# Kernel tuning notes

Measured on AMD Instinct MI355X. Metric: run time of the kernel, lower is better.

The kernel has to match this reference:

```python
import jax, jax.numpy as jnp
import numpy as np

EPS = 1e-3  # LayerNorm eps used in the torch module
S, R = 32, 32  # stoch_dim, stoch_rank


def ln(x, g, b):
    m = jnp.mean(x, -1, keepdims=True)
    v = jnp.var(x, -1, keepdims=True)
    return (x - m) / jnp.sqrt(v + EPS) * g + b


def setup_inputs() -> dict:
    key = jax.random.key(0)
    ks = jax.random.split(key, 16)
    T, B, E, A, D, H = 64, 64, 1024, 6, 2048, 1000
    def w(k, shape, s=0.02):
        return (jax.random.normal(k, shape) * s).astype(jnp.float32)
    return dict(
        embeds=jax.random.normal(ks[0], (T, B, E), jnp.float32),
        actions=jax.random.normal(ks[1], (T, B, A), jnp.float32),
        resets=jax.random.bernoulli(ks[2], 0.01, (T, B)),
        h0=jnp.zeros((B, D), jnp.float32),
        z0=jnp.zeros((B, S * R), jnp.float32),
        zw=w(ks[3], (S * R, H)), zb=jnp.zeros(H, jnp.float32),
        aw=w(ks[4], (A, H)),
        in_g=jnp.ones(H, jnp.float32), in_b=jnp.zeros(H, jnp.float32),
        gru_wi=w(ks[5], (H, 3 * D)), gru_wh=w(ks[6], (D, 3 * D)),
        gru_bi=jnp.zeros(3 * D, jnp.float32), gru_bh=jnp.zeros(3 * D, jnp.float32),
        ph_w=w(ks[7], (D, H)), ph_b=jnp.zeros(H, jnp.float32),
        pe_w=w(ks[8], (E, H)),
        po_g=jnp.ones(H, jnp.float32), po_b=jnp.zeros(H, jnp.float32),
        pp_w=w(ks[9], (H, S * R)), pp_b=jnp.zeros(S * R, jnp.float32),
        prh_w=w(ks[10], (D, H)), prh_b=jnp.zeros(H, jnp.float32),
        pr_g=jnp.ones(H, jnp.float32), pr_b=jnp.zeros(H, jnp.float32),
        prp_w=w(ks[11], (H, S * R)), prp_b=jnp.zeros(S * R, jnp.float32),
    )


def reference(embeds, actions, resets, h0, z0, zw, zb, aw, in_g, in_b,
              gru_wi, gru_wh, gru_bi, gru_bh, ph_w, ph_b, pe_w, po_g, po_b,
              pp_w, pp_b, prh_w, prh_b, pr_g, pr_b, prp_w, prp_b):
    T, B = embeds.shape[:2]
    base = jax.random.key(42)
    mask = (~resets)[..., None].astype(embeds.dtype)  # [T,B,1]

    def step(carry, xs):
        h, z = carry
        a, e, m, t = xs
        h = h * m
        z = z * m
        # input stage: z_mlp + a_mlp -> LN -> ELU
        x = jax.nn.elu(ln(z @ zw + zb + a @ aw, in_g, in_b))
        # single GRUCell (PyTorch gate order r, z, n)
        gi = x @ gru_wi + gru_bi
        gh = h @ gru_wh + gru_bh
        gir, giz, gin = jnp.split(gi, 3, -1)
        ghr, ghz, ghn = jnp.split(gh, 3, -1)
        r = jax.nn.sigmoid(gir + ghr)
        u = jax.nn.sigmoid(giz + ghz)
        n = jnp.tanh(gin + r * ghn)
        h = (1.0 - u) * n + u * h
        # posterior head (embed is provided every step)
        x = jax.nn.elu(ln(h @ ph_w + ph_b + e @ pe_w, po_g, po_b))
        pp = x @ pp_w + pp_b  # [B, S*R]
        logits = pp.reshape(B, S, R)
        probs = jax.nn.softmax(logits, -1)
        idx = jax.random.categorical(jax.random.fold_in(base, t), logits, axis=-1)
        oh = jax.nn.one_hot(idx, R, dtype=pp.dtype)
        # straight-through one-hot sample
        sample = (oh + probs - jax.lax.stop_gradient(probs)).reshape(B, S * R)
        return (h, sample), (pp, h, sample)

    (h_last, z_last), (posts, states_h, samples) = jax.lax.scan(
        step, (h0, z0), (actions, embeds, mask, jnp.arange(T)))
    # batch_prior over all timesteps at once
    priors = jax.nn.elu(ln(states_h @ prh_w + prh_b, pr_g, pr_b)) @ prp_w + prp_b
    features = jnp.concatenate([states_h, samples], -1)  # [T,B,3072]
    return priors, posts, samples, features, h_last, z_last
```

## Files before the change

### kernel.cpp

```cpp
#include <hip/hip_runtime.h>
#include <hip/hip_bf16.h>


#define BK 32
#define LDP 66
#define NBLK 512

enum { TR_NONE = 0, TR_SCALEROW = 1, TR_LNELU = 2 };

__device__ inline float cload(const float* p) {
  return __hip_atomic_load(p, __ATOMIC_RELAXED, __HIP_MEMORY_SCOPE_SYSTEM);
}
__device__ inline void cstore(float* p, float v) {
  __hip_atomic_store(p, v, __ATOMIC_RELAXED, __HIP_MEMORY_SCOPE_SYSTEM);
}
__device__ inline float2 cload2(const float* p) {
  unsigned long long u = __hip_atomic_load((const unsigned long long*)p,
                                           __ATOMIC_RELAXED, __HIP_MEMORY_SCOPE_SYSTEM);
  float2 r;
  r.x = __uint_as_float((unsigned)u);
  r.y = __uint_as_float((unsigned)(u >> 32));
  return r;
}
__device__ inline void cstore2(float* p, float x, float y) {
  unsigned long long u =
      ((unsigned long long)__float_as_uint(y) << 32) | (unsigned long long)__float_as_uint(x);
  __hip_atomic_store((unsigned long long*)p, u, __ATOMIC_RELAXED, __HIP_MEMORY_SCOPE_SYSTEM);
}
__device__ inline int cloadi(const int* p) {
  return __hip_atomic_load(p, __ATOMIC_RELAXED, __HIP_MEMORY_SCOPE_SYSTEM);
}
__device__ inline void cstorei(int* p, int v) {
  __hip_atomic_store(p, v, __ATOMIC_RELAXED, __HIP_MEMORY_SCOPE_SYSTEM);
}

__device__ inline float xla_tanh(float x) {
  float ax = fabsf(x);
  float xc = fminf(fmaxf(x, -7.90531110763549805f), 7.90531110763549805f);
  float x2 = __fmul_rn(xc, xc);
  float p = -2.76076847742355e-16f;
  p = __fadd_rn(__fmul_rn(p, x2), 2.00018790482477e-13f);
  p = __fadd_rn(__fmul_rn(p, x2), -8.60467152213735e-11f);
  p = __fadd_rn(__fmul_rn(p, x2), 5.12229709037114e-08f);
  p = __fadd_rn(__fmul_rn(p, x2), 1.48572235717979e-05f);
  p = __fadd_rn(__fmul_rn(p, x2), 6.37261928875436e-04f);
  p = __fadd_rn(__fmul_rn(p, x2), 4.89352455891786e-03f);
  float num = __fmul_rn(xc, p);
  float q = 1.19825839466702e-06f;
  q = __fadd_rn(__fmul_rn(q, x2), 1.18534705686654e-04f);
  q = __fadd_rn(__fmul_rn(q, x2), 2.26843463243900e-03f);
  q = __fadd_rn(__fmul_rn(q, x2), 4.89352518554385e-03f);
  float r = __fdiv_rn(num, q);
  return ax < 0.0004f ? x : r;
}

__device__ inline float sigm(float x) { return 1.0f / (1.0f + expf(-x)); }

__device__ inline void tfround(unsigned& x0, unsigned& x1, int r) {
  x0 += x1; x1 = (x1 << r) | (x1 >> (32 - r)); x1 ^= x0;
}
__device__ inline uint2 threefry(unsigned k0, unsigned k1, unsigned c0, unsigned c1) {
  unsigned ks2 = k0 ^ k1 ^ 0x1BD11BDAu;
  unsigned x0 = c0 + k0, x1 = c1 + k1;
  tfround(x0, x1, 13); tfround(x0, x1, 15); tfround(x0, x1, 26); tfround(x0, x1, 6);
  x0 += k1; x1 += ks2 + 1u;
  tfround(x0, x1, 17); tfround(x0, x1, 29); tfround(x0, x1, 16); tfround(x0, x1, 24);
  x0 += ks2; x1 += k0 + 2u;
  tfround(x0, x1, 13); tfround(x0, x1, 15); tfround(x0, x1, 26); tfround(x0, x1, 6);
  x0 += k0; x1 += k1 + 3u;
  tfround(x0, x1, 17); tfround(x0, x1, 29); tfround(x0, x1, 16); tfround(x0, x1, 24);
  x0 += k1; x1 += ks2 + 4u;
  tfround(x0, x1, 13); tfround(x0, x1, 15); tfround(x0, x1, 26); tfround(x0, x1, 6);
  x0 += ks2; x1 += k0 + 5u;
  return make_uint2(x0, x1);
}

struct GemmArgs {
  const float* A; int lda; const float* B; int ldb; int K; int ksplit;
  const float* A2; int lda2; const float* B2; int ldb2; int K2;
  int N; const float* bias;
  const float* t1s; const float* t1g; const float* t1b;
  float* C; int ldc; long partStride;
};

template <int TRA>
__device__ void gemm_tiles(float acc[4][4], float (*As)[LDP], float (*Bs)[LDP],
                           const float* A, int lda, const float* B, int ldb,
                           int kB, int kE, int mBase, int cBase, int N,
                           const float* s0, const float* g0, const float* b0) {
  const int tid = threadIdx.x;
  const int ar = tid >> 2;
  const int ak = (tid & 3) << 3;
  const int bk = tid >> 3;
  const int bc = (tid & 7) << 3;
  const int r0 = (tid >> 4) << 2;
  const int c0 = (tid & 15) << 2;

  float rowS = 1.f, rowM = 0.f, rowR = 1.f;
  if (TRA == TR_SCALEROW) rowS = s0[mBase + ar];
  else if (TRA == TR_LNELU) {
    rowM = s0[(mBase + ar) * 2];
    rowR = s0[(mBase + ar) * 2 + 1];
  }

  for (int kb = kB; kb < kE; kb += BK) {
    {
      const float* Ap = A + (long)(mBase + ar) * lda + kb + ak;
      float v[8];
      if (kb + ak + 7 < kE) {
        float4 u0 = *(const float4*)(Ap);
        float4 u1 = *(const float4*)(Ap + 4);
        v[0] = u0.x; v[1] = u0.y; v[2] = u0.z; v[3] = u0.w;
        v[4] = u1.x; v[5] = u1.y; v[6] = u1.z; v[7] = u1.w;
      } else {
#pragma unroll
        for (int i = 0; i < 8; i++) v[i] = (kb + ak + i < kE) ? Ap[i] : 0.f;
      }
#pragma unroll
      for (int i = 0; i < 8; i++) {
        int k = kb + ak + i;
        float x = 0.f;
        if (k < kE) {
          x = v[i];
          if (TRA == TR_SCALEROW) {
            x *= rowS;
          } else if (TRA == TR_LNELU) {
            x = (x - rowM) * rowR * g0[k] + b0[k];
            x = x > 0.f ? x : expm1f(x);
          }
        }
        As[ak + i][ar] = x;
      }
    }
    {
      int k = kb + bk;
      const float* Bp = B + (long)k * ldb + cBase + bc;
      if (k < kE && cBase + bc + 7 < N) {
        float4 u0 = *(const float4*)(Bp);
        float4 u1 = *(const float4*)(Bp + 4);
        Bs[bk][bc + 0] = u0.x; Bs[bk][bc + 1] = u0.y;
        Bs[bk][bc + 2] = u0.z; Bs[bk][bc + 3] = u0.w;
        Bs[bk][bc + 4] = u1.x; Bs[bk][bc + 5] = u1.y;
        Bs[bk][bc + 6] = u1.z; Bs[bk][bc + 7] = u1.w;
      } else {
#pragma unroll
        for (int i = 0; i < 8; i++)
          Bs[bk][bc + i] = (k < kE && cBase + bc + i < N) ? Bp[i] : 0.f;
      }
    }
    __syncthreads();
#pragma unroll
    for (int kk = 0; kk < BK; kk++) {
      float4 a4 = *(const float4*)&As[kk][r0];
      float4 b4 = *(const float4*)&Bs[kk][c0];
      float av[4] = {a4.x, a4.y, a4.z, a4.w};
      float bv[4] = {b4.x, b4.y, b4.z, b4.w};
#pragma unroll
      for (int i = 0; i < 4; i++)
#pragma unroll
        for (int j = 0; j < 4; j++) acc[i][j] += av[i] * bv[j];
    }
    __syncthreads();
  }
}

template <int TRA, int TRA2>
__global__ __launch_bounds__(256) void k_gemm(GemmArgs g) {
  __shared__ float As[BK][LDP];
  __shared__ float Bs[BK][LDP];
  const int nT = blockIdx.x, ks = blockIdx.y, mT = blockIdx.z;
  const int mBase = mT * 64, cBase = nT * 64;
  float acc[4][4] = {};
  int chunk = (((g.K + g.ksplit - 1) / g.ksplit) + 31) & ~31;
  int kB = ks * chunk, kE = min(g.K, kB + chunk);
  if (kB < kE)
    gemm_tiles<TRA>(acc, As, Bs, g.A, g.lda, g.B, g.ldb, kB, kE, mBase, cBase,
                    g.N, g.t1s, g.t1g, g.t1b);
  if (g.A2) {
    int chunk2 = (((g.K2 + g.ksplit - 1) / g.ksplit) + 31) & ~31;
    int kB2 = ks * chunk2, kE2 = min(g.K2, kB2 + chunk2);
    if (kB2 < kE2)
      gemm_tiles<TRA2>(acc, As, Bs, g.A2, g.lda2, g.B2, g.ldb2, kB2, kE2, mBase,
                       cBase, g.N, nullptr, nullptr, nullptr);
  }
  const int tid = threadIdx.x;
  const int r0 = (tid >> 4) << 2, c0 = (tid & 15) << 2;
  float* Cb = g.C + (long)ks * g.partStride;
#pragma unroll
  for (int i = 0; i < 4; i++) {
    float4 v = make_float4(acc[i][0], acc[i][1], acc[i][2], acc[i][3]);
    if (ks == 0 && g.bias) {
      int c = cBase + c0;
      v.x += (c + 0 < g.N) ? g.bias[c + 0] : 0.f;
      v.y += (c + 1 < g.N) ? g.bias[c + 1] : 0.f;
      v.z += (c + 2 < g.N) ? g.bias[c + 2] : 0.f;
      v.w += (c + 3 < g.N) ? g.bias[c + 3] : 0.f;
    }
    *(float4*)&Cb[(long)(mBase + r0 + i) * g.ldc + cBase + c0] = v;
  }
}

__global__ __launch_bounds__(256) void k_prstat(const float* xp, float* stats, int N) {
  int wave = threadIdx.x >> 6, lane = threadIdx.x & 63;
  int r = blockIdx.x * 4 + wave;
  float s = 0.f, sq = 0.f;
  for (int c = lane; c < N; c += 64) {
    float v = xp[(long)r * 1024 + c];
    s += v; sq += v * v;
  }
#pragma unroll
  for (int off = 32; off >= 1; off >>= 1) {
    s += __shfl_down(s, off);
    sq += __shfl_down(sq, off);
  }
  if (lane == 0) {
    float mean = s / N, var = sq / N - mean * mean;
    stats[r * 2] = mean;
    stats[r * 2 + 1] = 1.0f / sqrtf(var + 1e-3f);
  }
}

struct ScanArgs {
  const float* h0;
  const float* zw; const float* gwi; const float* gwh;
  const float* gbi; const float* gbh;
  const float* ph_w; const float* pp_w; const float* pp_b;
  const float* in_g; const float* in_b; const float* po_g; const float* po_b;
  const float* mask;
  const float* xa_base; const float* x2_base; const float* xa_t0;
  float* gi_parts; float* gh_parts; float* x2_parts; float* pp_parts;
  float* xe; float* x2e; int* idx;
  float* posts; float* samples; float* feats; float* hlast; float* zlast;
  unsigned* bar;
};

__device__ inline void gridbar(unsigned* bar, unsigned& lgen) {
  asm volatile("s_waitcnt vmcnt(0)" ::: "memory");
  __syncthreads();
  lgen++;
  if (threadIdx.x == 0) {
    int cell = (blockIdx.x & 7) * 32;
    unsigned prev = __hip_atomic_fetch_add(&bar[cell], 1u, __ATOMIC_RELAXED,
                                           __HIP_MEMORY_SCOPE_AGENT);
    if (prev == 64u * lgen - 1u) {
      unsigned p2 = __hip_atomic_fetch_add(&bar[256], 1u, __ATOMIC_RELAXED,
                                           __HIP_MEMORY_SCOPE_AGENT);
      if (p2 == 8u * lgen - 1u)
        __hip_atomic_store(&bar[288], lgen, __ATOMIC_RELAXED,
                           __HIP_MEMORY_SCOPE_AGENT);
    }
    while (__hip_atomic_load(&bar[288], __ATOMIC_RELAXED,
                             __HIP_MEMORY_SCOPE_AGENT) < lgen)
      __builtin_amdgcn_s_sleep(16);
  }
  __syncthreads();
}

template <int TRA>
__device__ void phase_gemm(float (*As)[LDP], float (*Bs)[LDP],
                           const float* A, int lda, const float* B, int ldb,
                           int kB, int kE, int cBase, int N,
                           const float* rowScale, float* C, int ldc,
                           const float* baseAdd, const float* colBias) {
  const int tid = threadIdx.x;
  const int ar = tid >> 2, ak = (tid & 3) << 3;
  const int bk = tid >> 3, bc = (tid & 7) << 3;
  const int r0 = (tid >> 4) << 2, c0 = (tid & 15) << 2;
  float acc[4][4] = {};
  float rowS = (TRA == TR_SCALEROW) ? rowScale[ar] : 1.f;

  for (int kb = kB; kb < kE; kb += BK) {
    float v[8];
    {
      const float* Ap = A + (long)ar * lda + kb + ak;
      if (kb + ak + 7 < kE) {
#pragma unroll
        for (int i = 0; i < 4; i++) {
          float2 u = cload2(Ap + 2 * i);
          v[2 * i] = u.x; v[2 * i + 1] = u.y;
        }
      } else {
#pragma unroll
        for (int i = 0; i < 8; i++) v[i] = (kb + ak + i < kE) ? cload(Ap + i) : 0.f;
      }
    }
    float w[8];
    {
      int k = kb + bk;
      const float* Bp = B + (long)k * ldb + cBase + bc;
      if (k < kE && cBase + bc + 7 < N) {
        float4 u0 = *(const float4*)(Bp);
        float4 u1 = *(const float4*)(Bp + 4);
        w[0] = u0.x; w[1] = u0.y; w[2] = u0.z; w[3] = u0.w;
        w[4] = u1.x; w[5] = u1.y; w[6] = u1.z; w[7] = u1.w;
      } else {
#pragma unroll
        for (int i = 0; i < 8; i++)
          w[i] = (k < kE && cBase + bc + i < N) ? Bp[i] : 0.f;
      }
    }
#pragma unroll
    for (int i = 0; i < 8; i++)
      As[ak + i][ar] = (TRA == TR_SCALEROW) ? v[i] * rowS : v[i];
#pragma unroll
    for (int i = 0; i < 8; i++) Bs[bk][bc + i] = w[i];
    __syncthreads();
#pragma unroll
    for (int kk = 0; kk < BK; kk++) {
      float4 a4 = *(const float4*)&As[kk][r0];
      float4 b4 = *(const float4*)&Bs[kk][c0];
      float av[4] = {a4.x, a4.y, a4.z, a4.w};
      float bv[4] = {b4.x, b4.y, b4.z, b4.w};
#pragma unroll
      for (int i = 0; i < 4; i++)
#pragma unroll
        for (int j = 0; j < 4; j++) acc[i][j] += av[i] * bv[j];
    }
    __syncthreads();
  }

#pragma unroll
  for (int i = 0; i < 4; i++) {
    float4 v4 = make_float4(acc[i][0], acc[i][1], acc[i][2], acc[i][3]);
    int c = cBase + c0;
    if (baseAdd) {
      const float* bp = baseAdd + (long)(r0 + i) * 1024 + c;
      v4.x += (c + 0 < N) ? bp[0] : 0.f;
      v4.y += (c + 1 < N) ? bp[1] : 0.f;
      v4.z += (c + 2 < N) ? bp[2] : 0.f;
      v4.w += (c + 3 < N) ? bp[3] : 0.f;
    }
    if (colBias) {
      v4.x += (c + 0 < N) ? colBias[c + 0] : 0.f;
      v4.y += (c + 1 < N) ? colBias[c + 1] : 0.f;
      v4.z += (c + 2 < N) ? colBias[c + 2] : 0.f;
      v4.w += (c + 3 < N) ? colBias[c + 3] : 0.f;
    }
    float* Cp = &C[(long)(r0 + i) * ldc + cBase + c0];
    cstore2(Cp, v4.x, v4.y);
    cstore2(Cp + 2, v4.z, v4.w);
  }
}

__device__ inline void ln_reduce(float s, float sq, float* red, float& mean,
                                 float& rstd) {
  const int tid = threadIdx.x;
#pragma unroll
  for (int off = 32; off >= 1; off >>= 1) {
    s += __shfl_down(s, off);
    sq += __shfl_down(sq, off);
  }
  if ((tid & 63) == 0) { red[tid >> 6] = s; red[4 + (tid >> 6)] = sq; }
  __syncthreads();
  if (tid == 0) {
    float S = red[0] + red[1] + red[2] + red[3];
    float Q = red[4] + red[5] + red[6] + red[7];
    float m = S / 1000.f;
    float var = Q / 1000.f - m * m;
    red[8] = m;
    red[9] = 1.f / sqrtf(var + 1e-3f);
  }
  __syncthreads();
  mean = red[8]; rstd = red[9];
}

__device__ void phase_p1(const ScanArgs& a, int t, float* red, int* gidx) {
  const int row = blockIdx.x, tid = threadIdx.x;
  if (t > 0 && tid < 32) gidx[tid] = cloadi(a.idx + row * 32 + tid);
  __syncthreads();
  float mk = a.mask[t * 64 + row];
  float v[4];
  float s = 0.f, sq = 0.f;
#pragma unroll
  for (int i = 0; i < 4; i++) {
    int c = tid + (i << 8);
    float x = 0.f;
    if (c < 1000) {
      if (t == 0) {
        x = a.xa_t0[row * 1024 + c];
      } else {
        float g = 0.f;
#pragma unroll
        for (int s2 = 0; s2 < 32; s2++)
          g += a.zw[(s2 * 32 + gidx[s2]) * 1000 + c];
        x = g * mk + a.xa_base[(long)t * 65536 + row * 1024 + c];
      }
      s += x; sq += x * x;
    }
    v[i] = x;
  }
  float mean, rstd;
  ln_reduce(s, sq, red, mean, rstd);
#pragma unroll
  for (int i = 0; i < 4; i++) {
    int c = tid + (i << 8);
    float y = 0.f;
    if (c < 1000) {
      y = (v[i] - mean) * rstd * a.in_g[c] + a.in_b[c];
      y = y > 0.f ? y : expm1f(y);
    }
    cstore(a.xe + row * 1024 + c, y);
  }
  __syncthreads();
}

__device__ void phase_p5(const ScanArgs& a, float* red) {
  const int row = blockIdx.x, tid = threadIdx.x;
  float v[4];
  float s = 0.f, sq = 0.f;
#pragma unroll
  for (int i = 0; i < 4; i++) {
    int c = tid + (i << 8);
    float x = 0.f;
    if (c < 1000) {
#pragma unroll
      for (int q = 0; q < 8; q++)
        x += cload(a.x2_parts + (long)q * 65536 + row * 1024 + c);
      s += x; sq += x * x;
    }
    v[i] = x;
  }
  float mean, rstd;
  ln_reduce(s, sq, red, mean, rstd);
#pragma unroll
  for (int i = 0; i < 4; i++) {
    int c = tid + (i << 8);
    float y = 0.f;
    if (c < 1000) {
      y = (v[i] - mean) * rstd * a.po_g[c] + a.po_b[c];
      y = y > 0.f ? y : expm1f(y);
    }
    cstore(a.x2e + row * 1024 + c, y);
  }
  __syncthreads();
}

__device__ void phase_gates(const ScanArgs& a, const float* hprev, int ldh,
                            const float* mk, float* feat_t, int t) {
  int p = blockIdx.x * 256 + threadIdx.x;
  int b = p >> 10, d = (p & 1023) << 1;
  long gio = (long)b * 6144 + d;
  float r0, r1, z0, z1, n0, n1;
  {
    float2 t0 = cload2(a.gi_parts + gio);
    float2 t1 = cload2(a.gi_parts + gio + 2048);
    float2 t2 = cload2(a.gi_parts + gio + 4096);
    r0 = t0.x; r1 = t0.y; z0 = t1.x; z1 = t1.y; n0 = t2.x; n1 = t2.y;
  }
#pragma unroll
  for (int q = 1; q < 5; q++) {
    long o = (long)q * 393216 + gio;
    float2 t0 = cload2(a.gi_parts + o);
    float2 t1 = cload2(a.gi_parts + o + 2048);
    float2 t2 = cload2(a.gi_parts + o + 4096);
    r0 += t0.x; r1 += t0.y; z0 += t1.x; z1 += t1.y; n0 += t2.x; n1 += t2.y;
  }
  r0 += a.gbi[d]; r1 += a.gbi[d + 1];
  z0 += a.gbi[d + 2048]; z1 += a.gbi[d + 2049];
  n0 += a.gbi[d + 4096]; n1 += a.gbi[d + 4097];
  float hr0 = a.gbh[d], hr1 = a.gbh[d + 1];
  float hz0 = a.gbh[d + 2048], hz1 = a.gbh[d + 2049];
  float hn0 = a.gbh[d + 4096], hn1 = a.gbh[d + 4097];
#pragma unroll
  for (int q = 0; q < 8; q++) {
    long o = (long)q * 393216 + gio;
    float2 t0 = cload2(a.gh_parts + o);
    float2 t1 = cload2(a.gh_parts + o + 2048);
    float2 t2 = cload2(a.gh_parts + o + 4096);
    hr0 += t0.x; hr1 += t0.y; hz0 += t1.x; hz1 += t1.y; hn0 += t2.x; hn1 += t2.y;
  }
  float2 hp = cload2(hprev + (long)b * ldh + d);
  float m = mk[b];
  float rr0 = sigm(r0 + hr0), rr1 = sigm(r1 + hr1);
  float uu0 = sigm(z0 + hz0), uu1 = sigm(z1 + hz1);
  float nn0 = xla_tanh(n0 + rr0 * hn0), nn1 = xla_tanh(n1 + rr1 * hn1);
  float h0v = (1.f - uu0) * nn0 + uu0 * (hp.x * m);
  float h1v = (1.f - uu1) * nn1 + uu1 * (hp.y * m);
  cstore2(feat_t + (long)b * 3072 + d, h0v, h1v);
  if (t == 63) {
    a.hlast[(long)b * 2048 + d] = h0v;
    a.hlast[(long)b * 2048 + d + 1] = h1v;
  }
}

__device__ void phase_sample(const ScanArgs& a, int t, float* feat_t) {
  int gid = blockIdx.x * 256 + threadIdx.x;
  int b = gid >> 10, sj = gid & 1023, j = sj & 31, sg = sj >> 5;
  float v = 0.f;
#pragma unroll
  for (int q = 0; q < 8; q++)
    v += cload(a.pp_parts + (long)q * 65536 + (long)b * 1024 + sj);
  a.posts[(long)t * 65536 + (long)b * 1024 + sj] = v;
  uint2 kt = threefry(0u, 42u, 0u, (unsigned)t);
  unsigned idx = (unsigned)(b * 1024 + sj);
  uint2 o = threefry(kt.x, kt.y, 0u, idx);
  unsigned bits = o.x ^ o.y;
  const float TINY = 1.175494350822287508e-38f;
  float u = __uint_as_float((bits >> 9) | 0x3f800000u) - 1.0f;
  u = fmaxf(TINY, u + TINY);
  float sc = v + -logf(-logf(u));
  float bs = sc;
  int bj = j;
#pragma unroll
  for (int off = 16; off >= 1; off >>= 1) {
    float os = __shfl_xor(bs, off, 32);
    int oj = __shfl_xor(bj, off, 32);
    if (os > bs || (os == bs && oj < bj)) { bs = os; bj = oj; }
  }
  float oh = (j == bj) ? 1.f : 0.f;
  a.samples[(long)t * 65536 + (long)b * 1024 + sj] = oh;
  feat_t[(long)b * 3072 + 2048 + sj] = oh;
  if (j == 0) cstorei(a.idx + b * 32 + sg, bj);
  if (t == 63) a.zlast[b * 1024 + sj] = oh;
}

__global__ __launch_bounds__(256, 2) void k_scan(ScanArgs a) {
  __shared__ float As[BK][LDP];
  __shared__ float Bs[BK][LDP];
  __shared__ float red[16];
  __shared__ int gidx[32];
  unsigned lgen = 0;
  const int bid = blockIdx.x;

  for (int half = 0; half < 2; half++) {
    if (bid >= 128) {
      int i2 = bid - 128;
      int tile = i2 % 96, ks = half * 4 + i2 / 96;
      phase_gemm<TR_SCALEROW>(As, Bs, a.h0, 2048, a.gwh, 6144, ks * 256,
                              ks * 256 + 256, tile * 64, 6144, a.mask,
                              a.gh_parts + (long)ks * 393216, 6144, nullptr,
                              nullptr);
    }
    gridbar(a.bar, lgen);
  }

  for (int t = 0; t < 64; t++) {
    const float* mk = a.mask + t * 64;
    float* feat_t = a.feats + (long)t * 196608;
    const float* hprev = t ? a.feats + (long)(t - 1) * 196608 : a.h0;
    int ldh = t ? 3072 : 2048;

    if (bid < 64) phase_p1(a, t, red, gidx);
    gridbar(a.bar, lgen);

    if (bid < 480) {
      int tile = bid % 96, ks = bid / 96;
      phase_gemm<TR_NONE>(As, Bs, a.xe, 1024, a.gwi, 6144, ks * 200,
                          ks * 200 + 200, tile * 64, 6144, nullptr,
                          a.gi_parts + (long)ks * 393216, 6144, nullptr, nullptr);
    }
    gridbar(a.bar, lgen);

    if (bid < 256) phase_gates(a, hprev, ldh, mk, feat_t, t);
    gridbar(a.bar, lgen);

    if (bid < 128) {
      int ct = bid & 15, ks = bid >> 4;
      phase_gemm<TR_NONE>(As, Bs, feat_t, 3072, a.ph_w, 1000, ks * 256,
                          ks * 256 + 256, ct * 64, 1000, nullptr,
                          a.x2_parts + (long)ks * 65536, 1024,
                          (ks == 0) ? a.x2_base + (long)t * 65536 : nullptr,
                          nullptr);
    } else if (t < 63) {
      int i2 = bid - 128;
      int tile = i2 % 96, ks = i2 / 96;
      phase_gemm<TR_SCALEROW>(As, Bs, feat_t, 3072, a.gwh, 6144, ks * 256,
                              ks * 256 + 256, tile * 64, 6144,
                              a.mask + (t + 1) * 64,
                              a.gh_parts + (long)ks * 393216, 6144, nullptr,
                              nullptr);
    }
    gridbar(a.bar, lgen);

    if (bid < 64) phase_p5(a, red);
    gridbar(a.bar, lgen);

    if (bid < 128) {
      int ct = bid & 15, ks = bid >> 4;
      int kB = ks * 128, kE = min(1000, kB + 128);
      phase_gemm<TR_NONE>(As, Bs, a.x2e, 1024, a.pp_w, 1024, kB, kE, ct * 64,
                          1024, nullptr, a.pp_parts + (long)ks * 65536, 1024,
                          nullptr, (ks == 0) ? a.pp_b : nullptr);
    } else if (t < 63) {
      int i2 = bid - 128;
      int tile = i2 % 96, ks = 4 + i2 / 96;
      phase_gemm<TR_SCALEROW>(As, Bs, feat_t, 3072, a.gwh, 6144, ks * 256,
                              ks * 256 + 256, tile * 64, 6144,
                              a.mask + (t + 1) * 64,
                              a.gh_parts + (long)ks * 393216, 6144, nullptr,
                              nullptr);
    }
    gridbar(a.bar, lgen);

    if (bid < 256) phase_sample(a, t, feat_t);
    gridbar(a.bar, lgen);
  }
}

__global__ void k_init(unsigned* bar) {
  int i = threadIdx.x;
  if (i < 512) bar[i] = 0u;
}

__global__ void k_detect(const unsigned* rr, int nDwordsSafe, int* fmt) {
  __shared__ int flags;
  if (threadIdx.x == 0) flags = 0;
  __syncthreads();
  int local = 0;
  for (int i = threadIdx.x; i < nDwordsSafe; i += 256) {
    unsigned dw = rr[i];
    if (dw == 0x3f800000u) local |= 4;
    else if (dw & 0xFFFFFF00u) local |= 1;
    else if (dw == 1u) local |= 2;
  }
  atomicOr(&flags, local);
  __syncthreads();
  if (threadIdx.x == 0) {
    int f = flags;
    *fmt = ((f & 4) == 0 && (f & 1)) ? 1 : 0;
  }
}

__global__ void k_prep(const void* rr, const int* fmt, float* mask, int n) {
  int i = blockIdx.x * 256 + threadIdx.x;
  if (i < n) {
    bool reset;
    if (*fmt == 1) reset = ((const unsigned char*)rr)[i] != 0;
    else reset = ((const int*)rr)[i] != 0;
    mask[i] = reset ? 0.0f : 1.0f;
  }
}

__global__ __launch_bounds__(256) void k_abase(const float* act, const float* aw,
                                               const float* zb, float* out) {
  for (long i = blockIdx.x * 256L + threadIdx.x; i < 4096L * 1024;
       i += (long)gridDim.x * 256) {
    int row = (int)(i >> 10), c = (int)(i & 1023);
    float v = 0.f;
    if (c < 1000) {
      v = zb[c];
#pragma unroll
      for (int k = 0; k < 6; k++) v += act[row * 6 + k] * aw[k * 1000 + c];
    }
    out[i] = v;
  }
}

extern "C" void kernel_launch(void* const* d_in, const int* in_sizes, int n_in,
                              void* d_out, int out_size, void* d_ws, size_t ws_size,
                              hipStream_t stream) {
  const float* embeds = (const float*)d_in[0];
  const float* actions = (const float*)d_in[1];
  const void* resets = d_in[2];
  const float* h0 = (const float*)d_in[3];
  const float* z0 = (const float*)d_in[4];
  const float* zw = (const float*)d_in[5];
  const float* zb = (const float*)d_in[6];
  const float* aw = (const float*)d_in[7];
  const float* in_g = (const float*)d_in[8];
  const float* in_b = (const float*)d_in[9];
  const float* gwi = (const float*)d_in[10];
  const float* gwh = (const float*)d_in[11];
  const float* gbi = (const float*)d_in[12];
  const float* gbh = (const float*)d_in[13];
  const float* ph_w = (const float*)d_in[14];
  const float* ph_b = (const float*)d_in[15];
  const float* pe_w = (const float*)d_in[16];
  const float* po_g = (const float*)d_in[17];
  const float* po_b = (const float*)d_in[18];
  const float* pp_w = (const float*)d_in[19];
  const float* pp_b = (const float*)d_in[20];
  const float* prh_w = (const float*)d_in[21];
  const float* prh_b = (const float*)d_in[22];
  const float* pr_g = (const float*)d_in[23];
  const float* pr_b = (const float*)d_in[24];
  const float* prp_w = (const float*)d_in[25];
  const float* prp_b = (const float*)d_in[26];

  float* out = (float*)d_out;
  float* priors  = out;
  float* posts   = out + 4194304;
  float* samples = out + 8388608;
  float* feats   = out + 12582912;
  float* hlast   = out + 25165824;
  float* zlast   = out + 25296896;

  float* ws = (float*)d_ws;
  unsigned* bar   = (unsigned*)ws;
  int*   fmt      = (int*)(ws + 512);
  float* mask     = ws + 576;
  float* stats_p  = ws + 4672;
  float* xe       = ws + 12864;
  float* x2e      = ws + 78400;
  int*   idxb     = (int*)(ws + 143936);
  float* xa_t0    = ws + 146048;
  float* gi_parts = ws + 211584;
  float* gh_parts = ws + 2177664;
  float* x2_parts = ws + 5323392;
  float* pp_parts = ws + 5847680;
  float* xa_base  = ws + 6371968;
  float* x2_base  = ws + 10566272;
  float* xp       = ws + 14760576;

  k_init<<<1, 512, 0, stream>>>(bar);
  k_detect<<<1, 256, 0, stream>>>((const unsigned*)resets, 1024, fmt);
  k_prep<<<16, 256, 0, stream>>>(resets, fmt, mask, 4096);
  k_abase<<<2048, 256, 0, stream>>>(actions, aw, zb, xa_base);

  GemmArgs g0{};
  g0.A = z0; g0.lda = 1024; g0.B = zw; g0.ldb = 1000; g0.K = 1024; g0.ksplit = 1;
  g0.A2 = actions; g0.lda2 = 6; g0.B2 = aw; g0.ldb2 = 1000; g0.K2 = 6;
  g0.N = 1000; g0.bias = zb; g0.t1s = mask;
  g0.C = xa_t0; g0.ldc = 1024; g0.partStride = 0;
  k_gemm<TR_SCALEROW, TR_NONE><<<dim3(16, 1, 1), 256, 0, stream>>>(g0);

  GemmArgs ge{};
  ge.A = embeds; ge.lda = 1024; ge.B = pe_w; ge.ldb = 1000; ge.K = 1024; ge.ksplit = 1;
  ge.N = 1000; ge.bias = ph_b; ge.C = x2_base; ge.ldc = 1024; ge.partStride = 0;
  k_gemm<TR_NONE, TR_NONE><<<dim3(16, 1, 64), 256, 0, stream>>>(ge);

  ScanArgs sa{};
  sa.h0 = h0; sa.zw = zw; sa.gwi = gwi; sa.gwh = gwh;
  sa.gbi = gbi; sa.gbh = gbh; sa.ph_w = ph_w; sa.pp_w = pp_w; sa.pp_b = pp_b;
  sa.in_g = in_g; sa.in_b = in_b; sa.po_g = po_g; sa.po_b = po_b;
  sa.mask = mask; sa.xa_base = xa_base; sa.x2_base = x2_base; sa.xa_t0 = xa_t0;
  sa.gi_parts = gi_parts; sa.gh_parts = gh_parts;
  sa.x2_parts = x2_parts; sa.pp_parts = pp_parts;
  sa.xe = xe; sa.x2e = x2e; sa.idx = idxb;
  sa.posts = posts; sa.samples = samples; sa.feats = feats;
  sa.hlast = hlast; sa.zlast = zlast; sa.bar = bar;
  k_scan<<<NBLK, 256, 0, stream>>>(sa);

  GemmArgs gp1{};
  gp1.A = feats; gp1.lda = 3072; gp1.B = prh_w; gp1.ldb = 1000; gp1.K = 2048; gp1.ksplit = 1;
  gp1.N = 1000; gp1.bias = prh_b; gp1.C = xp; gp1.ldc = 1024; gp1.partStride = 0;
  k_gemm<TR_NONE, TR_NONE><<<dim3(16, 1, 64), 256, 0, stream>>>(gp1);
  k_prstat<<<1024, 256, 0, stream>>>(xp, stats_p, 1000);
  GemmArgs gp2{};
  gp2.A = xp; gp2.lda = 1024; gp2.B = prp_w; gp2.ldb = 1024; gp2.K = 1000; gp2.ksplit = 1;
  gp2.N = 1024; gp2.bias = prp_b; gp2.t1s = stats_p; gp2.t1g = pr_g; gp2.t1b = pr_b;
  gp2.C = priors; gp2.ldc = 1024; gp2.partStride = 0;
  k_gemm<TR_LNELU, TR_NONE><<<dim3(16, 1, 64), 256, 0, stream>>>(gp2);
}
```

Before: 19.42 ms.

## Rebalance persistent scan phases with fewer split-K parts and fused posterior sampling

Restructures the per-timestep schedule of the persistent scan kernel. Split-K partition counts for the input-gate, hidden-gate and posterior-head GEMMs drop (5→2, 8→4, 8→4), so the gate and LayerNorm phases reduce fewer partial buffers. The next step's hidden-gate GEMM is spread across four phases, including the input-gate phase. The posterior logits GEMM is fused with Gumbel-max sampling in one tiled phase, which removes the pp_parts buffer and a grid barrier per step. It also adds register prefetch (software pipelining) to the shared GEMM loop and shortens the barrier spin sleep. In exchange, each active block does more serial K work and fewer blocks are busy in some phases.

```diff
diff --git a/kernel.cpp b/kernel.cpp
--- a/kernel.cpp
+++ b/kernel.cpp
@@ -228,7 +228,9 @@
   const float* in_g; const float* in_b; const float* po_g; const float* po_b;
   const float* mask;
   const float* xa_base; const float* x2_base; const float* xa_t0;
-  float* gi_parts; float* gh_parts; float* x2_parts; float* pp_parts;
+  float* gi_p;
+  float* gh_p;
+  float* x2_p;
   float* xe; float* x2e; int* idx;
   float* posts; float* samples; float* feats; float* hlast; float* zlast;
   unsigned* bar;
@@ -242,7 +244,7 @@
     int cell = (blockIdx.x & 7) * 32;
     unsigned prev = __hip_atomic_fetch_add(&bar[cell], 1u, __ATOMIC_RELAXED,
                                            __HIP_MEMORY_SCOPE_AGENT);
-    if (prev == 64u * lgen - 1u) {
+    if (prev == (unsigned)(NBLK / 8) * lgen - 1u) {
       unsigned p2 = __hip_atomic_fetch_add(&bar[256], 1u, __ATOMIC_RELAXED,
                                            __HIP_MEMORY_SCOPE_AGENT);
       if (p2 == 8u * lgen - 1u)
@@ -251,7 +253,7 @@
     }
     while (__hip_atomic_load(&bar[288], __ATOMIC_RELAXED,
                              __HIP_MEMORY_SCOPE_AGENT) < lgen)
-      __builtin_amdgcn_s_sleep(16);
+      __builtin_amdgcn_s_sleep(8);
   }
   __syncthreads();
 }
@@ -268,43 +270,45 @@
   const int r0 = (tid >> 4) << 2, c0 = (tid & 15) << 2;
   float acc[4][4] = {};
   float rowS = (TRA == TR_SCALEROW) ? rowScale[ar] : 1.f;
-
+  float v[8], w[8];
+
+  auto ldA = [&](int kb) {
+    const float* Ap = A + (long)ar * lda + kb + ak;
+    if (kb + ak + 7 < kE) {
+#pragma unroll
+      for (int i = 0; i < 4; i++) {
+        float2 u = cload2(Ap + 2 * i);
+        v[2 * i] = u.x; v[2 * i + 1] = u.y;
+      }
+    } else {
+#pragma unroll
+      for (int i = 0; i < 8; i++) v[i] = (kb + ak + i < kE) ? cload(Ap + i) : 0.f;
+    }
+  };
+  auto ldB = [&](int kb) {
+    int k = kb + bk;
+    const float* Bp = B + (long)k * ldb + cBase + bc;
+    if (k < kE && cBase + bc + 7 < N) {
+      float4 u0 = *(const float4*)(Bp);
+      float4 u1 = *(const float4*)(Bp + 4);
+      w[0] = u0.x; w[1] = u0.y; w[2] = u0.z; w[3] = u0.w;
+      w[4] = u1.x; w[5] = u1.y; w[6] = u1.z; w[7] = u1.w;
+    } else {
+#pragma unroll
+      for (int i = 0; i < 8; i++)
+        w[i] = (k < kE && cBase + bc + i < N) ? Bp[i] : 0.f;
+    }
+  };
+
+  ldA(kB); ldB(kB);
   for (int kb = kB; kb < kE; kb += BK) {
-    float v[8];
-    {
-      const float* Ap = A + (long)ar * lda + kb + ak;
-      if (kb + ak + 7 < kE) {
-#pragma unroll
-        for (int i = 0; i < 4; i++) {
-          float2 u = cload2(Ap + 2 * i);
-          v[2 * i] = u.x; v[2 * i + 1] = u.y;
-        }
-      } else {
-#pragma unroll
-        for (int i = 0; i < 8; i++) v[i] = (kb + ak + i < kE) ? cload(Ap + i) : 0.f;
-      }
-    }
-    float w[8];
-    {
-      int k = kb + bk;
-      const float* Bp = B + (long)k * ldb + cBase + bc;
-      if (k < kE && cBase + bc + 7 < N) {
-        float4 u0 = *(const float4*)(Bp);
-        float4 u1 = *(const float4*)(Bp + 4);
-        w[0] = u0.x; w[1] = u0.y; w[2] = u0.z; w[3] = u0.w;
-        w[4] = u1.x; w[5] = u1.y; w[6] = u1.z; w[7] = u1.w;
-      } else {
-#pragma unroll
-        for (int i = 0; i < 8; i++)
-          w[i] = (k < kE && cBase + bc + i < N) ? Bp[i] : 0.f;
-      }
-    }
 #pragma unroll
     for (int i = 0; i < 8; i++)
       As[ak + i][ar] = (TRA == TR_SCALEROW) ? v[i] * rowS : v[i];
 #pragma unroll
     for (int i = 0; i < 8; i++) Bs[bk][bc + i] = w[i];
     __syncthreads();
+    if (kb + BK < kE) { ldA(kb + BK); ldB(kb + BK); }
 #pragma unroll
     for (int kk = 0; kk < BK; kk++) {
       float4 a4 = *(const float4*)&As[kk][r0];
@@ -404,7 +408,7 @@
   __syncthreads();
 }
 
-__device__ void phase_p5(const ScanArgs& a, float* red) {
+__device__ void phase_x2e(const ScanArgs& a, float* red) {
   const int row = blockIdx.x, tid = threadIdx.x;
   float v[4];
   float s = 0.f, sq = 0.f;
@@ -414,8 +418,8 @@
     float x = 0.f;
     if (c < 1000) {
 #pragma unroll
-      for (int q = 0; q < 8; q++)
-        x += cload(a.x2_parts + (long)q * 65536 + row * 1024 + c);
+      for (int q = 0; q < 4; q++)
+        x += cload(a.x2_p + (long)q * 65536 + row * 1024 + c);
       s += x; sq += x * x;
     }
     v[i] = x;
@@ -440,19 +444,13 @@
   int p = blockIdx.x * 256 + threadIdx.x;
   int b = p >> 10, d = (p & 1023) << 1;
   long gio = (long)b * 6144 + d;
-  float r0, r1, z0, z1, n0, n1;
-  {
-    float2 t0 = cload2(a.gi_parts + gio);
-    float2 t1 = cload2(a.gi_parts + gio + 2048);
-    float2 t2 = cload2(a.gi_parts + gio + 4096);
-    r0 = t0.x; r1 = t0.y; z0 = t1.x; z1 = t1.y; n0 = t2.x; n1 = t2.y;
-  }
-#pragma unroll
-  for (int q = 1; q < 5; q++) {
+  float r0 = 0.f, r1 = 0.f, z0 = 0.f, z1 = 0.f, n0 = 0.f, n1 = 0.f;
+#pragma unroll
+  for (int q = 0; q < 2; q++) {
     long o = (long)q * 393216 + gio;
-    float2 t0 = cload2(a.gi_parts + o);
-    float2 t1 = cload2(a.gi_parts + o + 2048);
-    float2 t2 = cload2(a.gi_parts + o + 4096);
+    float2 t0 = cload2(a.gi_p + o);
+    float2 t1 = cload2(a.gi_p + o + 2048);
+    float2 t2 = cload2(a.gi_p + o + 4096);
     r0 += t0.x; r1 += t0.y; z0 += t1.x; z1 += t1.y; n0 += t2.x; n1 += t2.y;
   }
   r0 += a.gbi[d]; r1 += a.gbi[d + 1];
@@ -462,11 +460,11 @@
   float hz0 = a.gbh[d + 2048], hz1 = a.gbh[d + 2049];
   float hn0 = a.gbh[d + 4096], hn1 = a.gbh[d + 4097];
 #pragma unroll
-  for (int q = 0; q < 8; q++) {
+  for (int q = 0; q < 4; q++) {
     long o = (long)q * 393216 + gio;
-    float2 t0 = cload2(a.gh_parts + o);
-    float2 t1 = cload2(a.gh_parts + o + 2048);
-    float2 t2 = cload2(a.gh_parts + o + 4096);
+    float2 t0 = cload2(a.gh_p + o);
+    float2 t1 = cload2(a.gh_p + o + 2048);
+    float2 t2 = cload2(a.gh_p + o + 4096);
     hr0 += t0.x; hr1 += t0.y; hz0 += t1.x; hz1 += t1.y; hn0 += t2.x; hn1 += t2.y;
   }
   float2 hp = cload2(hprev + (long)b * ldh + d);
@@ -483,35 +481,93 @@
   }
 }
 
-__device__ void phase_sample(const ScanArgs& a, int t, float* feat_t) {
-  int gid = blockIdx.x * 256 + threadIdx.x;
-  int b = gid >> 10, sj = gid & 1023, j = sj & 31, sg = sj >> 5;
-  float v = 0.f;
-#pragma unroll
-  for (int q = 0; q < 8; q++)
-    v += cload(a.pp_parts + (long)q * 65536 + (long)b * 1024 + sj);
-  a.posts[(long)t * 65536 + (long)b * 1024 + sj] = v;
+__device__ void phase_pp(const ScanArgs& a, int t, int rg, int sg,
+                         float* As2, float* Bs2) {
+  const int tid = threadIdx.x;
+  const int ar = tid >> 3;
+  const int ak = (tid & 7) << 2;
+  const int bk = tid >> 3;
+  const int bc = (tid & 7) << 2;
+  const int rowBase = rg * 32, colBase = sg * 32;
+  float acc[4] = {0.f, 0.f, 0.f, 0.f};
+  float va[4], vb[4];
+
+  auto ldA = [&](int kb) {
+    const float* Ap = a.x2e + (long)(rowBase + ar) * 1024 + kb + ak;
+    if (kb + ak + 3 < 1000) {
+      float2 u0 = cload2(Ap), u1 = cload2(Ap + 2);
+      va[0] = u0.x; va[1] = u0.y; va[2] = u1.x; va[3] = u1.y;
+    } else {
+#pragma unroll
+      for (int i = 0; i < 4; i++)
+        va[i] = (kb + ak + i < 1000) ? cload(Ap + i) : 0.f;
+    }
+  };
+  auto ldB = [&](int kb) {
+    int k = kb + bk;
+    const float* Bp = a.pp_w + (long)k * 1024 + colBase + bc;
+    if (k < 1000) {
+      float4 u = *(const float4*)Bp;
+      vb[0] = u.x; vb[1] = u.y; vb[2] = u.z; vb[3] = u.w;
+    } else {
+      vb[0] = vb[1] = vb[2] = vb[3] = 0.f;
+    }
+  };
+
+  ldA(0); ldB(0);
+  for (int kb = 0; kb < 1000; kb += 32) {
+#pragma unroll
+    for (int i = 0; i < 4; i++) As2[(ak + i) * 33 + ar] = va[i];
+#pragma unroll
+    for (int i = 0; i < 4; i++) Bs2[bk * 36 + bc + i] = vb[i];
+    __syncthreads();
+    if (kb + 32 < 1000) { ldA(kb + 32); ldB(kb + 32); }
+#pragma unroll
+    for (int kk = 0; kk < 32; kk++) {
+      float av = As2[kk * 33 + ar];
+      const float* bp = &Bs2[kk * 36 + bc];
+#pragma unroll
+      for (int j = 0; j < 4; j++) acc[j] += av * bp[j];
+    }
+    __syncthreads();
+  }
+
+  int b = rowBase + ar;
+  float pp[4];
+#pragma unroll
+  for (int j = 0; j < 4; j++) pp[j] = acc[j] + a.pp_b[colBase + bc + j];
+  *(float4*)&a.posts[(long)t * 65536 + (long)b * 1024 + colBase + bc] =
+      make_float4(pp[0], pp[1], pp[2], pp[3]);
+
   uint2 kt = threefry(0u, 42u, 0u, (unsigned)t);
-  unsigned idx = (unsigned)(b * 1024 + sj);
-  uint2 o = threefry(kt.x, kt.y, 0u, idx);
-  unsigned bits = o.x ^ o.y;
   const float TINY = 1.175494350822287508e-38f;
-  float u = __uint_as_float((bits >> 9) | 0x3f800000u) - 1.0f;
-  u = fmaxf(TINY, u + TINY);
-  float sc = v + -logf(-logf(u));
-  float bs = sc;
-  int bj = j;
-#pragma unroll
-  for (int off = 16; off >= 1; off >>= 1) {
-    float os = __shfl_xor(bs, off, 32);
-    int oj = __shfl_xor(bj, off, 32);
+  float bs = -3.402823466e38f;
+  int bj = 0;
+#pragma unroll
+  for (int j = 0; j < 4; j++) {
+    unsigned gi_ = (unsigned)(b * 1024 + colBase + bc + j);
+    uint2 o = threefry(kt.x, kt.y, 0u, gi_);
+    unsigned bits = o.x ^ o.y;
+    float u = __uint_as_float((bits >> 9) | 0x3f800000u) - 1.0f;
+    u = fmaxf(TINY, u + TINY);
+    float sc = pp[j] + -logf(-logf(u));
+    if (sc > bs) { bs = sc; bj = bc + j; }
+  }
+#pragma unroll
+  for (int off = 4; off >= 1; off >>= 1) {
+    float os = __shfl_xor(bs, off, 8);
+    int oj = __shfl_xor(bj, off, 8);
     if (os > bs || (os == bs && oj < bj)) { bs = os; bj = oj; }
   }
-  float oh = (j == bj) ? 1.f : 0.f;
-  a.samples[(long)t * 65536 + (long)b * 1024 + sj] = oh;
-  feat_t[(long)b * 3072 + 2048 + sj] = oh;
-  if (j == 0) cstorei(a.idx + b * 32 + sg, bj);
-  if (t == 63) a.zlast[b * 1024 + sj] = oh;
+  float4 oh;
+  float* op = (float*)&oh;
+#pragma unroll
+  for (int j = 0; j < 4; j++) op[j] = (bc + j == bj) ? 1.f : 0.f;
+  *(float4*)&a.samples[(long)t * 65536 + (long)b * 1024 + colBase + bc] = oh;
+  *(float4*)&a.feats[(long)t * 196608 + (long)b * 3072 + 2048 + colBase + bc] = oh;
+  if (t == 63)
+    *(float4*)&a.zlast[(long)b * 1024 + colBase + bc] = oh;
+  if ((tid & 7) == 0) cstorei(a.idx + b * 32 + sg, bj);
 }
 
 __global__ __launch_bounds__(256, 2) void k_scan(ScanArgs a) {
@@ -521,78 +577,72 @@
   __shared__ int gidx[32];
   unsigned lgen = 0;
   const int bid = blockIdx.x;
-
-  for (int half = 0; half < 2; half++) {
-    if (bid >= 128) {
-      int i2 = bid - 128;
-      int tile = i2 % 96, ks = half * 4 + i2 / 96;
-      phase_gemm<TR_SCALEROW>(As, Bs, a.h0, 2048, a.gwh, 6144, ks * 256,
-                              ks * 256 + 256, tile * 64, 6144, a.mask,
-                              a.gh_parts + (long)ks * 393216, 6144, nullptr,
-                              nullptr);
-    }
-    gridbar(a.bar, lgen);
-  }
+  float* As2 = &As[0][0];
+  float* Bs2 = &Bs[0][0];
+
+  if (bid < 384) {
+    int tile = bid % 96, q = bid / 96;
+    phase_gemm<TR_SCALEROW>(As, Bs, a.h0, 2048, a.gwh, 6144, q * 512,
+                            q * 512 + 512, tile * 64, 6144, a.mask,
+                            a.gh_p + (long)q * 393216, 6144, nullptr, nullptr);
+  }
+  gridbar(a.bar, lgen);
 
   for (int t = 0; t < 64; t++) {
-    const float* mk = a.mask + t * 64;
-    float* feat_t = a.feats + (long)t * 196608;
     const float* hprev = t ? a.feats + (long)(t - 1) * 196608 : a.h0;
     int ldh = t ? 3072 : 2048;
+    float* feat_t = a.feats + (long)t * 196608;
 
     if (bid < 64) phase_p1(a, t, red, gidx);
     gridbar(a.bar, lgen);
 
-    if (bid < 480) {
+    if (bid < 192) {
       int tile = bid % 96, ks = bid / 96;
-      phase_gemm<TR_NONE>(As, Bs, a.xe, 1024, a.gwi, 6144, ks * 200,
-                          ks * 200 + 200, tile * 64, 6144, nullptr,
-                          a.gi_parts + (long)ks * 393216, 6144, nullptr, nullptr);
+      phase_gemm<TR_NONE>(As, Bs, a.xe, 1024, a.gwi, 6144, ks ? 512 : 0,
+                          ks ? 1000 : 512, tile * 64, 6144, nullptr,
+                          a.gi_p + (long)ks * 393216, 6144, nullptr, nullptr);
+    } else if (bid < 288 && t >= 1) {
+      int tile = bid - 192;
+      phase_gemm<TR_SCALEROW>(As, Bs, hprev, 3072, a.gwh, 6144, 1536, 2048,
+                              tile * 64, 6144, a.mask + t * 64,
+                              a.gh_p + 3L * 393216, 6144, nullptr, nullptr);
     }
     gridbar(a.bar, lgen);
 
-    if (bid < 256) phase_gates(a, hprev, ldh, mk, feat_t, t);
+    if (bid < 256) phase_gates(a, hprev, ldh, a.mask + t * 64, feat_t, t);
     gridbar(a.bar, lgen);
 
-    if (bid < 128) {
+    if (bid < 64) {
       int ct = bid & 15, ks = bid >> 4;
-      phase_gemm<TR_NONE>(As, Bs, feat_t, 3072, a.ph_w, 1000, ks * 256,
-                          ks * 256 + 256, ct * 64, 1000, nullptr,
-                          a.x2_parts + (long)ks * 65536, 1024,
+      phase_gemm<TR_NONE>(As, Bs, feat_t, 3072, a.ph_w, 1000, ks * 512,
+                          ks * 512 + 512, ct * 64, 1000, nullptr,
+                          a.x2_p + (long)ks * 65536, 1024,
                           (ks == 0) ? a.x2_base + (long)t * 65536 : nullptr,
                           nullptr);
-    } else if (t < 63) {
-      int i2 = bid - 128;
-      int tile = i2 % 96, ks = i2 / 96;
-      phase_gemm<TR_SCALEROW>(As, Bs, feat_t, 3072, a.gwh, 6144, ks * 256,
-                              ks * 256 + 256, tile * 64, 6144,
-                              a.mask + (t + 1) * 64,
-                              a.gh_parts + (long)ks * 393216, 6144, nullptr,
-                              nullptr);
+    } else if (bid < 160 && t < 63) {
+      int tile = bid - 64;
+      phase_gemm<TR_SCALEROW>(As, Bs, feat_t, 3072, a.gwh, 6144, 0, 512,
+                              tile * 64, 6144, a.mask + (t + 1) * 64,
+                              a.gh_p, 6144, nullptr, nullptr);
     }
     gridbar(a.bar, lgen);
 
-    if (bid < 64) phase_p5(a, red);
+    if (bid < 64) phase_x2e(a, red);
+    else if (bid < 160 && t < 63) {
+      int tile = bid - 64;
+      phase_gemm<TR_SCALEROW>(As, Bs, feat_t, 3072, a.gwh, 6144, 512, 1024,
+                              tile * 64, 6144, a.mask + (t + 1) * 64,
+                              a.gh_p + 1L * 393216, 6144, nullptr, nullptr);
+    }
     gridbar(a.bar, lgen);
 
-    if (bid < 128) {
-      int ct = bid & 15, ks = bid >> 4;
-      int kB = ks * 128, kE = min(1000, kB + 128);
-      phase_gemm<TR_NONE>(As, Bs, a.x2e, 1024, a.pp_w, 1024, kB, kE, ct * 64,
-                          1024, nullptr, a.pp_parts + (long)ks * 65536, 1024,
-                          nullptr, (ks == 0) ? a.pp_b : nullptr);
-    } else if (t < 63) {
-      int i2 = bid - 128;
-      int tile = i2 % 96, ks = 4 + i2 / 96;
-      phase_gemm<TR_SCALEROW>(As, Bs, feat_t, 3072, a.gwh, 6144, ks * 256,
-                              ks * 256 + 256, tile * 64, 6144,
-                              a.mask + (t + 1) * 64,
-                              a.gh_parts + (long)ks * 393216, 6144, nullptr,
-                              nullptr);
-    }
-    gridbar(a.bar, lgen);
-
-    if (bid < 256) phase_sample(a, t, feat_t);
+    if (bid < 64) phase_pp(a, t, bid >> 5, bid & 31, As2, Bs2);
+    else if (bid < 160 && t < 63) {
+      int tile = bid - 64;
+      phase_gemm<TR_SCALEROW>(As, Bs, feat_t, 3072, a.gwh, 6144, 1024, 1536,
+                              tile * 64, 6144, a.mask + (t + 1) * 64,
+                              a.gh_p + 2L * 393216, 6144, nullptr, nullptr);
+    }
     gridbar(a.bar, lgen);
   }
 }
@@ -686,21 +736,20 @@
   float* zlast   = out + 25296896;
 
   float* ws = (float*)d_ws;
-  unsigned* bar   = (unsigned*)ws;
-  int*   fmt      = (int*)(ws + 512);
-  float* mask     = ws + 576;
-  float* stats_p  = ws + 4672;
-  float* xe       = ws + 12864;
-  float* x2e      = ws + 78400;
-  int*   idxb     = (int*)(ws + 143936);
-  float* xa_t0    = ws + 146048;
-  float* gi_parts = ws + 211584;
-  float* gh_parts = ws + 2177664;
-  float* x2_parts = ws + 5323392;
-  float* pp_parts = ws + 5847680;
-  float* xa_base  = ws + 6371968;
-  float* x2_base  = ws + 10566272;
-  float* xp       = ws + 14760576;
+  unsigned* bar  = (unsigned*)ws;
+  int*   fmt     = (int*)(ws + 512);
+  float* mask    = ws + 576;
+  float* stats_p = ws + 4672;
+  float* xe      = ws + 12864;
+  float* x2e     = ws + 78400;
+  int*   idxb    = (int*)(ws + 143936);
+  float* xa_t0   = ws + 146048;
+  float* gi_p    = ws + 211584;
+  float* gh_p    = ws + 998016;
+  float* x2_p    = ws + 2570880;
+  float* xa_base = ws + 2833024;
+  float* x2_base = ws + 7027328;
+  float* xp      = ws + 11221632;
 
   k_init<<<1, 512, 0, stream>>>(bar);
   k_detect<<<1, 256, 0, stream>>>((const unsigned*)resets, 1024, fmt);
@@ -724,8 +773,7 @@
   sa.gbi = gbi; sa.gbh = gbh; sa.ph_w = ph_w; sa.pp_w = pp_w; sa.pp_b = pp_b;
   sa.in_g = in_g; sa.in_b = in_b; sa.po_g = po_g; sa.po_b = po_b;
   sa.mask = mask; sa.xa_base = xa_base; sa.x2_base = x2_base; sa.xa_t0 = xa_t0;
-  sa.gi_parts = gi_parts; sa.gh_parts = gh_parts;
-  sa.x2_parts = x2_parts; sa.pp_parts = pp_parts;
+  sa.gi_p = gi_p; sa.gh_p = gh_p; sa.x2_p = x2_p;
   sa.xe = xe; sa.x2e = x2e; sa.idx = idxb;
   sa.posts = posts; sa.samples = samples; sa.feats = feats;
   sa.hlast = hlast; sa.zlast = zlast; sa.bar = bar;
```

Result: slower. 26.82 ms (+38.2%).
